# Kernel tuning notes

Hardware: AMD Instinct MI355X
Metric: run time of the kernel (lower is better)

## Reference

```python
import jax, jax.numpy as jnp
import numpy as np

HID = 768
INTER = 3072
H = 12
DH = 64
N = 16384
W = 256   # attention_width
L = 512   # per-sequence length (power of 2, used via the uint32 bit-mask trick)


def rotate_every_two(x):
    x1 = x[..., ::2]
    x2 = x[..., 1::2]
    return jnp.stack((-x2, x1), axis=-1).reshape(x.shape)


def setup_inputs() -> dict:
    key = jax.random.key(0)
    ks = jax.random.split(key, 6)
    # GPT-J style interleaved rotary tables: sin/cos each value repeated twice
    inv_freq = 1.0 / (10000.0 ** (np.arange(0, DH, 2) / DH))  # [DH/2]
    ang = np.arange(N)[:, None] * inv_freq[None, :]           # [N, DH/2]
    pos_sin = jnp.asarray(np.repeat(np.sin(ang), 2, axis=-1), dtype=jnp.float32)
    pos_cos = jnp.asarray(np.repeat(np.cos(ang), 2, axis=-1), dtype=jnp.float32)
    return {
        "x": jax.random.normal(ks[0], (N, HID), dtype=jnp.float32),
        "normed_ages": jax.random.normal(ks[1], (N,), dtype=jnp.float32),
        "pos_sin": pos_sin,
        "pos_cos": pos_cos,
        "ln_scale": jnp.ones((HID,), dtype=jnp.float32),
        "ln_offset": jnp.zeros((HID,), dtype=jnp.float32),
        "w_in": jax.random.normal(ks[2], (HID, 3 * HID + INTER), dtype=jnp.float32) * 0.02,
        "b_in": jnp.zeros((3 * HID + INTER,), dtype=jnp.float32),
        "w_out": jax.random.normal(ks[3], (HID + INTER, HID), dtype=jnp.float32) * 0.02,
        "b_out": jnp.zeros((HID,), dtype=jnp.float32),
        "length": L,
    }


def reference(x, normed_ages, pos_sin, pos_cos, ln_scale, ln_offset,
              w_in, b_in, w_out, b_out, length):
    # LayerNorm (haiku: eps=1e-5, create_scale/offset)
    mu = jnp.mean(x, axis=-1, keepdims=True)
    var = jnp.var(x, axis=-1, keepdims=True)
    xn = (x - mu) * jax.lax.rsqrt(var + 1e-5) * ln_scale + ln_offset

    # fused QKV + FF projection (note: original computes x_with_ages but never uses it)
    mid = xn @ w_in + b_in
    q, k, v, ff = jnp.split(mid, [HID, 2 * HID, 3 * HID], axis=-1)

    def to_heads(t):  # [N, HID] -> [H, N, DH]
        return t.reshape(N, H, DH).transpose(1, 0, 2)

    q, k, v = to_heads(q), to_heads(k), to_heads(v)

    # rotary ('per_head'): sincos broadcast over heads
    sin, cos = pos_sin[None], pos_cos[None]
    q = q * cos + rotate_every_two(q) * sin
    k = k * cos + rotate_every_two(k) * sin

    # local (sliding-window, causal, within-sequence) attention, chunked by W
    C = W
    nc = N // C
    qc = q.reshape(H, nc, C, DH)
    kc = k.reshape(H, nc, C, DH)
    vc = v.reshape(H, nc, C, DH)
    kprev = jnp.concatenate([jnp.zeros_like(kc[:, :1]), kc[:, :-1]], axis=1)
    vprev = jnp.concatenate([jnp.zeros_like(vc[:, :1]), vc[:, :-1]], axis=1)
    kcat = jnp.concatenate([kprev, kc], axis=2)  # [H, nc, 2C, DH]
    vcat = jnp.concatenate([vprev, vc], axis=2)

    qi = (jnp.arange(nc) * C)[:, None] + jnp.arange(C)        # [nc, C]
    kj = (jnp.arange(nc) * C)[:, None] - C + jnp.arange(2 * C)  # [nc, 2C]
    lm = ~(jnp.uint32(length) - jnp.uint32(1))  # same bit-trick as the module
    same_seq = ((qi[:, :, None].astype(jnp.uint32) & lm) ==
                (jnp.maximum(kj, 0)[:, None, :].astype(jnp.uint32) & lm))
    d = qi[:, :, None] - kj[:, None, :]
    mask = (kj[:, None, :] >= 0) & (d >= 0) & (d < W) & same_seq  # [nc, C, 2C]

    scale = 1.0 / jnp.sqrt(jnp.float32(DH))
    scores = jnp.einsum('hncd,hnkd->hnck', qc, kcat) * scale
    scores = jnp.where(mask[None], scores, jnp.float32(-1e30))
    probs = jax.nn.softmax(scores, axis=-1)
    attn = jnp.einsum('hnck,hnkd->hncd', probs, vcat)

    attn = attn.reshape(H, N, DH).transpose(1, 0, 2).reshape(N, HID)
    combined = jnp.concatenate([attn, jax.nn.gelu(ff)], axis=-1)
    return xn + combined @ w_out + b_out
```

## Files before the change

kernel.cpp:

```cpp
#include <hip/hip_runtime.h>

#define N_TOK 16384
#define HIDN  768
#define MIDN  5376
#define COMBN 3840
#define NH    12
#define DHD   64
#define CHUNK 256
#define WIN   256

typedef short s16x8 __attribute__((ext_vector_type(8)));
typedef short s16x4 __attribute__((ext_vector_type(4)));
typedef float f32x4 __attribute__((ext_vector_type(4)));

__device__ __forceinline__ float bf2f(unsigned short u){
  union { unsigned u; float f; } x; x.u = ((unsigned)u) << 16; return x.f;
}
__device__ __forceinline__ unsigned short f2bf(float f){
  union { float f; unsigned u; } x; x.f = f;
  unsigned r = x.u + 0x7fffu + ((x.u >> 16) & 1u);
  return (unsigned short)(r >> 16);
}
__device__ __forceinline__ float gelu_fast(float x){
  float u = -1.5957691216057308f * (x + 0.044715f * x * x * x);
  return x / (1.f + __expf(u));
}
__device__ __forceinline__ void glds16(const void* g, void* l){
  __builtin_amdgcn_global_load_lds(
      (const __attribute__((address_space(1))) unsigned*)g,
      (__attribute__((address_space(3))) unsigned*)l, 16, 0, 0);
}

__global__ __launch_bounds__(256) void transpose_f2b(
    const float* __restrict__ in, unsigned short* __restrict__ out,
    int R, int Cc)
{
  __shared__ short t[64 * 72];
  const int tid = threadIdx.x;
  const int r0 = blockIdx.y * 64, c0 = blockIdx.x * 64;
  #pragma unroll
  for (int rep = 0; rep < 4; rep++){
    int v = tid + 256 * rep;
    int r = v >> 4, s = v & 15;
    float4 d = *(const float4*)(in + (size_t)(r0 + r) * Cc + c0 + s * 4);
    s16x4 o = { (short)f2bf(d.x), (short)f2bf(d.y), (short)f2bf(d.z), (short)f2bf(d.w) };
    *(s16x4*)(t + r * 72 + s * 4) = o;
  }
  __syncthreads();
  #pragma unroll
  for (int rep = 0; rep < 2; rep++){
    int v = tid + 256 * rep;
    int c = v & 63, s2 = v >> 6;
    s16x8 d;
    #pragma unroll
    for (int j = 0; j < 8; j++) d[j] = t[(s2 * 8 + j) * 72 + c];
    *(s16x8*)(out + (size_t)(c0 + c) * R + r0 + s2 * 8) = d;
  }
}

__global__ __launch_bounds__(256) void ln_kernel(
    const float* __restrict__ x, const float* __restrict__ sc,
    const float* __restrict__ ofs, unsigned short* __restrict__ xn)
{
  const int lane = threadIdx.x & 63, wv = threadIdx.x >> 6;
  const int row = blockIdx.x * 4 + wv;
  const float4* xr = (const float4*)(x + (size_t)row * HIDN);
  float4 vals[3];
  float sum = 0.f, sq = 0.f;
  #pragma unroll
  for (int j = 0; j < 3; j++){
    vals[j] = xr[lane + 64 * j];
    sum += vals[j].x + vals[j].y + vals[j].z + vals[j].w;
    sq  += vals[j].x * vals[j].x + vals[j].y * vals[j].y
         + vals[j].z * vals[j].z + vals[j].w * vals[j].w;
  }
  #pragma unroll
  for (int o = 1; o < 64; o <<= 1){ sum += __shfl_xor(sum, o); sq += __shfl_xor(sq, o); }
  const float mu = sum * (1.f / HIDN);
  const float rs = rsqrtf(fmaxf(sq * (1.f / HIDN) - mu * mu, 0.f) + 1e-5f);
  s16x4* xo = (s16x4*)(xn + (size_t)row * HIDN);
  const float4* scp = (const float4*)sc;
  const float4* ofp = (const float4*)ofs;
  #pragma unroll
  for (int j = 0; j < 3; j++){
    int p = lane + 64 * j;
    float4 s = scp[p], o = ofp[p];
    s16x4 w;
    w[0] = (short)f2bf((vals[j].x - mu) * rs * s.x + o.x);
    w[1] = (short)f2bf((vals[j].y - mu) * rs * s.y + o.y);
    w[2] = (short)f2bf((vals[j].z - mu) * rs * s.z + o.z);
    w[3] = (short)f2bf((vals[j].w - mu) * rs * s.w + o.w);
    xo[p] = w;
  }
}

template<int K>
__device__ __forceinline__ void gemm_tile128(
    const unsigned short* __restrict__ A, const unsigned short* __restrict__ BT,
    short* As, short* Bs,
    int tid, int quad, int l15, int wr, int wc, int m0, int n0,
    f32x4 acc[4][4])
{
  constexpr int T = K / 32;
  const int srow = tid >> 2;
  const int ksw  = ((tid & 3) ^ ((tid >> 3) & 3)) * 8;
  const unsigned short* Ap = A  + (size_t)(m0 + srow) * K + ksw;
  const unsigned short* Bp = BT + (size_t)(n0 + srow) * K + ksw;
  const size_t hstep = (size_t)64 * K;
  char* Ad = ((char*)As) + tid * 16;
  char* Bd = ((char*)Bs) + tid * 16;

  const int seg = ((quad ^ ((l15 >> 1) & 3)) << 4);
  int offA[4], offB[4];
  #pragma unroll
  for (int mf = 0; mf < 4; mf++) offA[mf] = (wr * 64 + mf * 16 + l15) * 64 + seg;
  #pragma unroll
  for (int nf = 0; nf < 4; nf++) offB[nf] = (wc * 64 + nf * 16 + l15) * 64 + seg;

  for (int t = 0; t < T; t++){
    __syncthreads();
    glds16(Ap + t * 32,         Ad);
    glds16(Ap + t * 32 + hstep, Ad + 4096);
    glds16(Bp + t * 32,         Bd);
    glds16(Bp + t * 32 + hstep, Bd + 4096);
    __syncthreads();
    s16x8 a[4], b[4];
    #pragma unroll
    for (int i = 0; i < 4; i++) a[i] = *(const s16x8*)(((const char*)As) + offA[i]);
    #pragma unroll
    for (int j = 0; j < 4; j++) b[j] = *(const s16x8*)(((const char*)Bs) + offB[j]);
    #pragma unroll
    for (int i = 0; i < 4; i++)
      #pragma unroll
      for (int j = 0; j < 4; j++)
        acc[i][j] = __builtin_amdgcn_mfma_f32_16x16x32_bf16(a[i], b[j], acc[i][j], 0, 0, 0);
  }
}

__global__ __launch_bounds__(256, 3) void gemm1_k(
    const unsigned short* __restrict__ A, const unsigned short* __restrict__ BT,
    const float* __restrict__ bias,
    unsigned short* __restrict__ qb, unsigned short* __restrict__ kb,
    unsigned short* __restrict__ vb, unsigned short* __restrict__ comb)
{
  __shared__ short As[128 * 32];
  __shared__ short Bs[128 * 32];
  const int tid = threadIdx.x, lane = tid & 63, wv = tid >> 6;
  const int quad = lane >> 4, l15 = lane & 15;
  const int wr = wv >> 1, wc = wv & 1;

  const int nbx = gridDim.x;
  const int bid = blockIdx.x + blockIdx.y * nbx;
  const int GM = 16;
  const int group = bid / (GM * nbx);
  const int rem   = bid % (GM * nbx);
  const int m0 = (group * GM + (rem % GM)) * 128;
  const int n0 = (rem / GM) * 128;

  f32x4 acc[4][4];
  #pragma unroll
  for (int i = 0; i < 4; i++)
    #pragma unroll
    for (int j = 0; j < 4; j++) acc[i][j] = (f32x4){0.f,0.f,0.f,0.f};

  gemm_tile128<HIDN>(A, BT, As, Bs, tid, quad, l15, wr, wc, m0, n0, acc);

  unsigned short* dstb; int cb; bool isff = false;
  if (n0 < 768)       { dstb = qb;   cb = n0; }
  else if (n0 < 1536) { dstb = kb;   cb = n0 - 768; }
  else if (n0 < 2304) { dstb = vb;   cb = n0 - 1536; }
  else                { dstb = comb; cb = n0 - 1536; isff = true; }
  const int rowstride = isff ? COMBN : HIDN;

  float bsv[4];
  #pragma unroll
  for (int nf = 0; nf < 4; nf++) bsv[nf] = bias[n0 + wc * 64 + nf * 16 + l15];

  #pragma unroll
  for (int mf = 0; mf < 4; mf++){
    #pragma unroll
    for (int r = 0; r < 4; r++){
      const int row = m0 + wr * 64 + mf * 16 + quad * 4 + r;
      unsigned short* rp = dstb + (size_t)row * rowstride + cb + wc * 64;
      #pragma unroll
      for (int nf = 0; nf < 4; nf++){
        float val = acc[mf][nf][r] + bsv[nf];
        if (isff) val = gelu_fast(val);
        rp[nf * 16 + l15] = f2bf(val);
      }
    }
  }
}

__global__ __launch_bounds__(256, 3) void gemm2_k(
    const unsigned short* __restrict__ A, const unsigned short* __restrict__ BT,
    const float* __restrict__ bias, const unsigned short* __restrict__ xn,
    float* __restrict__ outp)
{
  __shared__ short As[128 * 32];
  __shared__ short Bs[128 * 32];
  const int tid = threadIdx.x, lane = tid & 63, wv = tid >> 6;
  const int quad = lane >> 4, l15 = lane & 15;
  const int wr = wv >> 1, wc = wv & 1;
  const int n0 = blockIdx.x * 128, m0 = blockIdx.y * 128;

  f32x4 acc[4][4];
  #pragma unroll
  for (int i = 0; i < 4; i++)
    #pragma unroll
    for (int j = 0; j < 4; j++) acc[i][j] = (f32x4){0.f,0.f,0.f,0.f};

  gemm_tile128<COMBN>(A, BT, As, Bs, tid, quad, l15, wr, wc, m0, n0, acc);

  float bsv[4];
  #pragma unroll
  for (int nf = 0; nf < 4; nf++) bsv[nf] = bias[n0 + wc * 64 + nf * 16 + l15];

  #pragma unroll
  for (int mf = 0; mf < 4; mf++){
    #pragma unroll
    for (int r = 0; r < 4; r++){
      const int row = m0 + wr * 64 + mf * 16 + quad * 4 + r;
      const size_t rb = (size_t)row * HIDN + n0 + wc * 64;
      #pragma unroll
      for (int nf = 0; nf < 4; nf++){
        const size_t o = rb + nf * 16 + l15;
        outp[o] = bf2f(xn[o]) + acc[mf][nf][r] + bsv[nf];
      }
    }
  }
}

__global__ __launch_bounds__(384) void rope_qk(
    unsigned short* __restrict__ qb, unsigned short* __restrict__ kb,
    const float* __restrict__ psin, const float* __restrict__ pcos)
{
  __shared__ float ss[2048], cs[2048];
  const int tid = threadIdx.x, g = blockIdx.x;
  #pragma unroll
  for (int rep = 0; rep < 6; rep++){
    int idx = rep * 384 + tid;
    if (idx < 2048){
      int tok = idx >> 5, p = idx & 31;
      size_t gt = ((size_t)(g * 64 + tok)) * DHD + 2 * p;
      ss[idx] = psin[gt];
      cs[idx] = pcos[gt];
    }
  }
  __syncthreads();
  const int p = tid & 31;
  unsigned* q32 = (unsigned*)qb;
  unsigned* k32 = (unsigned*)kb;
  for (int tok = 0; tok < 64; tok++){
    const size_t a = ((size_t)(g * 64 + tok)) * 384 + tid;
    const float s = ss[tok * 32 + p], c0 = cs[tok * 32 + p];
    unsigned u = q32[a];
    float e = bf2f((unsigned short)(u & 0xffff));
    float d = bf2f((unsigned short)(u >> 16));
    q32[a] = (unsigned)f2bf((e * c0 - d * s) * 0.125f)
           | (((unsigned)f2bf((d * c0 + e * s) * 0.125f)) << 16);
    u = k32[a];
    e = bf2f((unsigned short)(u & 0xffff));
    d = bf2f((unsigned short)(u >> 16));
    k32[a] = (unsigned)f2bf(e * c0 - d * s)
           | (((unsigned)f2bf(d * c0 + e * s)) << 16);
  }
}

__global__ __launch_bounds__(256) void attn_kernel(
    const unsigned short* __restrict__ qb, const unsigned short* __restrict__ kb,
    const unsigned short* __restrict__ vb, unsigned short* __restrict__ comb,
    const int* __restrict__ lenp)
{
  __shared__ short Ks[2][64 * 72];
  __shared__ short Vt[2][64 * 64];
  __shared__ short Ps[4][16 * 72];
  const int tid = threadIdx.x, lane = tid & 63, wv = tid >> 6;
  const int quad = lane >> 4, l15 = lane & 15;
  const int h = blockIdx.y, c = blockIdx.x;
  const unsigned lm = ~((unsigned)lenp[0] - 1u);
  const int i0 = c * CHUNK + wv * 64;
  const unsigned short* qh = qb + h * DHD;
  const unsigned short* kh = kb + h * DHD;
  const unsigned short* vh = vb + h * DHD;

  s16x8 qf[4][2];
  #pragma unroll
  for (int rt = 0; rt < 4; rt++){
    const unsigned short* qr = qh + (size_t)(i0 + rt * 16 + l15) * HIDN;
    qf[rt][0] = *(const s16x8*)(qr + quad * 8);
    qf[rt][1] = *(const s16x8*)(qr + 32 + quad * 8);
  }

  f32x4 O[4][4];
  float mm[4][4], ll[4][4];
  #pragma unroll
  for (int rt = 0; rt < 4; rt++)
    #pragma unroll
    for (int j = 0; j < 4; j++){ O[rt][j] = (f32x4){0,0,0,0}; mm[rt][j] = -1e30f; ll[rt][j] = 0.f; }
  short* myP = &Ps[wv][0];

  const int skey = tid & 63, sseg = tid >> 6;
  const int jb0 = c * CHUNK - 256;
  s16x8 kr[2], vr[2];

  auto issue = [&](int jb){
    if (jb >= 0){
      const unsigned short* kp = kh + (size_t)(jb + skey) * HIDN + sseg * 16;
      const unsigned short* vp = vh + (size_t)(jb + skey) * HIDN + sseg * 16;
      kr[0] = *(const s16x8*)(kp);     kr[1] = *(const s16x8*)(kp + 8);
      vr[0] = *(const s16x8*)(vp);     vr[1] = *(const s16x8*)(vp + 8);
    } else {
      kr[0] = kr[1] = vr[0] = vr[1] = (s16x8){0,0,0,0,0,0,0,0};
    }
  };

  issue(jb0);
  for (int tb = 0; tb < 8; tb++){
    const int jb = jb0 + tb * 64;
    const int buf = tb & 1;
    short* Kb = &Ks[buf][0];
    short* Vb = &Vt[buf][0];
    *(s16x8*)(Kb + skey * 72 + sseg * 16)     = kr[0];
    *(s16x8*)(Kb + skey * 72 + sseg * 16 + 8) = kr[1];
    #pragma unroll
    for (int half = 0; half < 2; half++)
      #pragma unroll
      for (int j = 0; j < 8; j++){
        const int d = sseg * 16 + half * 8 + j;
        Vb[d * 64 + (((skey & 56) ^ ((d & 7) << 3)) | (skey & 7))] = vr[half][j];
      }
    if (tb < 7) issue(jb + 64);
    __syncthreads();

    const bool act = (jb >= 0) && (jb <= i0 + 63) && (jb + 63 >= i0 - 255) &&
                     (((unsigned)i0 & lm) == ((unsigned)jb & lm));
    if (!act) continue;

    #pragma unroll
    for (int rt = 0; rt < 4; rt++){
      const int ilo = i0 + rt * 16;
      if (ilo + 15 < jb || ilo - (jb + 63) >= WIN) continue;
      f32x4 sc[4];
      #pragma unroll
      for (int ct = 0; ct < 4; ct++){
        const short* kbase = Kb + (ct * 16 + l15) * 72 + quad * 8;
        const s16x8 b0 = *(const s16x8*)(kbase);
        const s16x8 b1 = *(const s16x8*)(kbase + 32);
        f32x4 aa = (f32x4){0,0,0,0};
        aa = __builtin_amdgcn_mfma_f32_16x16x32_bf16(qf[rt][0], b0, aa, 0, 0, 0);
        aa = __builtin_amdgcn_mfma_f32_16x16x32_bf16(qf[rt][1], b1, aa, 0, 0, 0);
        sc[ct] = aa;
      }
      float alph[4];
      #pragma unroll
      for (int r = 0; r < 4; r++){
        const int i = ilo + quad * 4 + r;
        #pragma unroll
        for (int ct = 0; ct < 4; ct++){
          const unsigned dd = (unsigned)(i - (jb + ct * 16 + l15));
          if (dd >= 256u) sc[ct][r] = -1e30f;
        }
        float mx = fmaxf(fmaxf(sc[0][r], sc[1][r]), fmaxf(sc[2][r], sc[3][r]));
        mx = fmaxf(mx, __shfl_xor(mx, 1));
        mx = fmaxf(mx, __shfl_xor(mx, 2));
        mx = fmaxf(mx, __shfl_xor(mx, 4));
        mx = fmaxf(mx, __shfl_xor(mx, 8));
        const float mnew = fmaxf(mm[rt][r], mx);
        alph[r] = __expf(mm[rt][r] - mnew);
        mm[rt][r] = mnew;
        float p0 = __expf(sc[0][r] - mnew);
        float p1 = __expf(sc[1][r] - mnew);
        float p2 = __expf(sc[2][r] - mnew);
        float p3 = __expf(sc[3][r] - mnew);
        sc[0][r] = p0; sc[1][r] = p1; sc[2][r] = p2; sc[3][r] = p3;
        float rsum = (p0 + p1) + (p2 + p3);
        rsum += __shfl_xor(rsum, 1);
        rsum += __shfl_xor(rsum, 2);
        rsum += __shfl_xor(rsum, 4);
        rsum += __shfl_xor(rsum, 8);
        ll[rt][r] = ll[rt][r] * alph[r] + rsum;
      }
      #pragma unroll
      for (int co = 0; co < 4; co++)
        #pragma unroll
        for (int r = 0; r < 4; r++) O[rt][co][r] *= alph[r];
      #pragma unroll
      for (int r = 0; r < 4; r++){
        const int prow = quad * 4 + r;
        #pragma unroll
        for (int ct = 0; ct < 4; ct++)
          myP[prow * 72 + ct * 16 + l15] = (short)f2bf(sc[ct][r]);
      }
      #pragma unroll
      for (int ks2 = 0; ks2 < 2; ks2++){
        const s16x8 pf = *(const s16x8*)(myP + l15 * 72 + ks2 * 32 + quad * 8);
        #pragma unroll
        for (int co = 0; co < 4; co++){
          const int d = co * 16 + l15;
          const s16x8 vf = *(const s16x8*)(Vb + d * 64 +
                              ((ks2 * 32 + quad * 8) ^ ((d & 7) << 3)));
          O[rt][co] = __builtin_amdgcn_mfma_f32_16x16x32_bf16(pf, vf, O[rt][co], 0, 0, 0);
        }
      }
    }
  }

  #pragma unroll
  for (int rt = 0; rt < 4; rt++)
    #pragma unroll
    for (int co = 0; co < 4; co++)
      #pragma unroll
      for (int r = 0; r < 4; r++){
        const int tok = i0 + rt * 16 + quad * 4 + r;
        comb[(size_t)tok * COMBN + h * DHD + co * 16 + l15] = f2bf(O[rt][co][r] / ll[rt][r]);
      }
}

extern "C" void kernel_launch(void* const* d_in, const int* in_sizes, int n_in,
                              void* d_out, int out_size, void* d_ws, size_t ws_size,
                              hipStream_t stream)
{
  const float* x     = (const float*)d_in[0];
  const float* psin  = (const float*)d_in[2];
  const float* pcos  = (const float*)d_in[3];
  const float* lns   = (const float*)d_in[4];
  const float* lno   = (const float*)d_in[5];
  const float* w_in  = (const float*)d_in[6];
  const float* b_in  = (const float*)d_in[7];
  const float* w_out = (const float*)d_in[8];
  const float* b_out = (const float*)d_in[9];
  const int*   lenp  = (const int*)d_in[10];
  float* out = (float*)d_out;

  char* ws = (char*)d_ws;
  size_t off = 0;
  unsigned short* xn    = (unsigned short*)(ws + off); off += (size_t)N_TOK * HIDN * 2;
  unsigned short* wInT  = (unsigned short*)(ws + off); off += (size_t)MIDN * HIDN * 2;
  unsigned short* wOutT = (unsigned short*)(ws + off); off += (size_t)HIDN * COMBN * 2;
  unsigned short* qbuf  = (unsigned short*)(ws + off); off += (size_t)N_TOK * HIDN * 2;
  unsigned short* kbuf  = (unsigned short*)(ws + off); off += (size_t)N_TOK * HIDN * 2;
  unsigned short* vbuf  = (unsigned short*)(ws + off); off += (size_t)N_TOK * HIDN * 2;
  unsigned short* comb  = (unsigned short*)(ws + off); off += (size_t)N_TOK * COMBN * 2;

  transpose_f2b<<<dim3(MIDN/64, HIDN/64), 256, 0, stream>>>(w_in, wInT, HIDN, MIDN);
  transpose_f2b<<<dim3(HIDN/64, COMBN/64), 256, 0, stream>>>(w_out, wOutT, COMBN, HIDN);
  ln_kernel<<<dim3(N_TOK/4), 256, 0, stream>>>(x, lns, lno, xn);
  gemm1_k<<<dim3(MIDN/128, N_TOK/128), 256, 0, stream>>>(
      xn, wInT, b_in, qbuf, kbuf, vbuf, comb);
  rope_qk<<<dim3(N_TOK/64), 384, 0, stream>>>(qbuf, kbuf, psin, pcos);
  attn_kernel<<<dim3(N_TOK/CHUNK, NH), 256, 0, stream>>>(
      qbuf, kbuf, vbuf, comb, lenp);
  gemm2_k<<<dim3(HIDN/128, N_TOK/128), 256, 0, stream>>>(
      comb, wOutT, b_out, xn, out);
}
```

Baseline: 626.7 us.

## Double-buffer GEMM LDS tiles with async global-to-LDS prefetch and MFMA priority

Replaces the single-buffered K=32 GEMM main loop with a two-stage pipeline over K=64 tiles, each split into two 32-wide halves. The loads for the next tile are issued into the alternate LDS buffer while MFMAs run on the current one, with explicit vmcnt waits and raw s_barrier instead of two __syncthreads per step. MFMA sections are wrapped in raised s_setprio. Shared memory grows to 64 KB per block and launch bounds drop from 3 to 2 blocks per CU, trading occupancy for latency hiding.

New measurement: 613.7 us. 2.1% less time.

```diff
diff --git a/kernel.cpp b/kernel.cpp
--- a/kernel.cpp
+++ b/kernel.cpp
@@ -95,56 +95,90 @@
 }
 
 template<int K>
-__device__ __forceinline__ void gemm_tile128(
+__device__ __forceinline__ void gemm_pipe2(
     const unsigned short* __restrict__ A, const unsigned short* __restrict__ BT,
-    short* As, short* Bs,
+    short* SM,
     int tid, int quad, int l15, int wr, int wc, int m0, int n0,
     f32x4 acc[4][4])
 {
-  constexpr int T = K / 32;
+  constexpr int T = K / 64;
+  char* const SMc = (char*)SM;
   const int srow = tid >> 2;
   const int ksw  = ((tid & 3) ^ ((tid >> 3) & 3)) * 8;
   const unsigned short* Ap = A  + (size_t)(m0 + srow) * K + ksw;
   const unsigned short* Bp = BT + (size_t)(n0 + srow) * K + ksw;
-  const size_t hstep = (size_t)64 * K;
-  char* Ad = ((char*)As) + tid * 16;
-  char* Bd = ((char*)Bs) + tid * 16;
-
-  const int seg = ((quad ^ ((l15 >> 1) & 3)) << 4);
+  const size_t rstep = (size_t)64 * K;
+
+  const int segx = ((quad ^ ((l15 >> 1) & 3)) << 4);
   int offA[4], offB[4];
   #pragma unroll
-  for (int mf = 0; mf < 4; mf++) offA[mf] = (wr * 64 + mf * 16 + l15) * 64 + seg;
-  #pragma unroll
-  for (int nf = 0; nf < 4; nf++) offB[nf] = (wc * 64 + nf * 16 + l15) * 64 + seg;
-
-  for (int t = 0; t < T; t++){
-    __syncthreads();
-    glds16(Ap + t * 32,         Ad);
-    glds16(Ap + t * 32 + hstep, Ad + 4096);
-    glds16(Bp + t * 32,         Bd);
-    glds16(Bp + t * 32 + hstep, Bd + 4096);
-    __syncthreads();
-    s16x8 a[4], b[4];
-    #pragma unroll
-    for (int i = 0; i < 4; i++) a[i] = *(const s16x8*)(((const char*)As) + offA[i]);
-    #pragma unroll
-    for (int j = 0; j < 4; j++) b[j] = *(const s16x8*)(((const char*)Bs) + offB[j]);
+  for (int mf = 0; mf < 4; mf++) offA[mf] = (wr * 64 + mf * 16 + l15) * 64 + segx;
+  #pragma unroll
+  for (int nf = 0; nf < 4; nf++) offB[nf] = (wc * 64 + nf * 16 + l15) * 64 + segx;
+
+  auto stage = [&](int tt, int kh, int b){
+    const int coff = tt * 64 + kh * 32;
+    char* Ad = SMc + b * 32768 + kh * 8192 + tid * 16;
+    char* Bd = SMc + b * 32768 + 16384 + kh * 8192 + tid * 16;
+    glds16(Ap + coff,         Ad);
+    glds16(Ap + coff + rstep, Ad + 4096);
+    glds16(Bp + coff,         Bd);
+    glds16(Bp + coff + rstep, Bd + 4096);
+  };
+
+  s16x8 af[4], bf[4];
+  auto rdfrags = [&](int b, int kh){
+    const char* Ab = SMc + b * 32768 + kh * 8192;
+    const char* Bb = SMc + b * 32768 + 16384 + kh * 8192;
+    #pragma unroll
+    for (int i = 0; i < 4; i++) af[i] = *(const s16x8*)(Ab + offA[i]);
+    #pragma unroll
+    for (int j = 0; j < 4; j++) bf[j] = *(const s16x8*)(Bb + offB[j]);
+  };
+
+  stage(0, 0, 0);
+  stage(0, 1, 0);
+  asm volatile("s_waitcnt vmcnt(4)" ::: "memory");
+  asm volatile("s_barrier" ::: "memory");
+  rdfrags(0, 0);
+
+  for (int t = 0; t < T; ++t){
+    const int cur = t & 1;
+    if (t + 1 < T) stage(t + 1, 0, cur ^ 1);
+    __builtin_amdgcn_s_setprio(1);
     #pragma unroll
     for (int i = 0; i < 4; i++)
       #pragma unroll
       for (int j = 0; j < 4; j++)
-        acc[i][j] = __builtin_amdgcn_mfma_f32_16x16x32_bf16(a[i], b[j], acc[i][j], 0, 0, 0);
-  }
-}
-
-__global__ __launch_bounds__(256, 3) void gemm1_k(
+        acc[i][j] = __builtin_amdgcn_mfma_f32_16x16x32_bf16(af[i], bf[j], acc[i][j], 0, 0, 0);
+    __builtin_amdgcn_s_setprio(0);
+    if (t + 1 < T){ asm volatile("s_waitcnt vmcnt(4)" ::: "memory"); }
+    else          { asm volatile("s_waitcnt vmcnt(0)" ::: "memory"); }
+    asm volatile("s_barrier" ::: "memory");
+    rdfrags(cur, 1);
+    if (t + 1 < T) stage(t + 1, 1, cur ^ 1);
+    __builtin_amdgcn_s_setprio(1);
+    #pragma unroll
+    for (int i = 0; i < 4; i++)
+      #pragma unroll
+      for (int j = 0; j < 4; j++)
+        acc[i][j] = __builtin_amdgcn_mfma_f32_16x16x32_bf16(af[i], bf[j], acc[i][j], 0, 0, 0);
+    __builtin_amdgcn_s_setprio(0);
+    if (t + 1 < T){
+      asm volatile("s_waitcnt vmcnt(4)" ::: "memory");
+      asm volatile("s_barrier" ::: "memory");
+      rdfrags(cur ^ 1, 0);
+    }
+  }
+}
+
+__global__ __launch_bounds__(256, 2) void gemm1_k(
     const unsigned short* __restrict__ A, const unsigned short* __restrict__ BT,
     const float* __restrict__ bias,
     unsigned short* __restrict__ qb, unsigned short* __restrict__ kb,
     unsigned short* __restrict__ vb, unsigned short* __restrict__ comb)
 {
-  __shared__ short As[128 * 32];
-  __shared__ short Bs[128 * 32];
+  __shared__ short SM[32768];
   const int tid = threadIdx.x, lane = tid & 63, wv = tid >> 6;
   const int quad = lane >> 4, l15 = lane & 15;
   const int wr = wv >> 1, wc = wv & 1;
@@ -163,7 +197,7 @@
     #pragma unroll
     for (int j = 0; j < 4; j++) acc[i][j] = (f32x4){0.f,0.f,0.f,0.f};
 
-  gemm_tile128<HIDN>(A, BT, As, Bs, tid, quad, l15, wr, wc, m0, n0, acc);
+  gemm_pipe2<HIDN>(A, BT, SM, tid, quad, l15, wr, wc, m0, n0, acc);
 
   unsigned short* dstb; int cb; bool isff = false;
   if (n0 < 768)       { dstb = qb;   cb = n0; }
@@ -192,13 +226,12 @@
   }
 }
 
-__global__ __launch_bounds__(256, 3) void gemm2_k(
+__global__ __launch_bounds__(256, 2) void gemm2_k(
     const unsigned short* __restrict__ A, const unsigned short* __restrict__ BT,
     const float* __restrict__ bias, const unsigned short* __restrict__ xn,
     float* __restrict__ outp)
 {
-  __shared__ short As[128 * 32];
-  __shared__ short Bs[128 * 32];
+  __shared__ short SM[32768];
   const int tid = threadIdx.x, lane = tid & 63, wv = tid >> 6;
   const int quad = lane >> 4, l15 = lane & 15;
   const int wr = wv >> 1, wc = wv & 1;
@@ -210,7 +243,7 @@
     #pragma unroll
     for (int j = 0; j < 4; j++) acc[i][j] = (f32x4){0.f,0.f,0.f,0.f};
 
-  gemm_tile128<COMBN>(A, BT, As, Bs, tid, quad, l15, wr, wc, m0, n0, acc);
+  gemm_pipe2<COMBN>(A, BT, SM, tid, quad, l15, wr, wc, m0, n0, acc);
 
   float bsv[4];
   #pragma unroll
```
